# Performance work log

Measured on AMD Instinct MI355X. Metric: run time of the kernel, lower is better.

The kernel has to match this reference:

```python
import jax, jax.numpy as jnp
import numpy as np

L1, L2, N, C = 4096, 4096, 8, 3


def setup_inputs() -> dict:
    key = jax.random.key(0)
    k1, k2 = jax.random.split(key)
    coords1 = jax.random.uniform(k1, (L1, N, C), dtype=jnp.float32)
    coords2 = jax.random.uniform(k2, (L2, N, C), dtype=jnp.float32)
    return {"coords1": coords1, "coords2": coords2}


def reference(coords1, coords2):
    # coords1: [L1, N, C], coords2: [L2, N, C]
    l1, n, c = coords1.shape
    l2 = coords2.shape[0]
    # Batch-first layout, matching flatten_batch semantics (per-batch NN only)
    q = jnp.swapaxes(coords2, 0, 1)  # [N, L2, C] query points
    r = jnp.swapaxes(coords1, 0, 1)  # [N, L1, C] reference points
    # Squared euclidean distances per batch: [N, L2, L1]
    d2 = (
        jnp.sum(q * q, axis=-1)[:, :, None]
        + jnp.sum(r * r, axis=-1)[:, None, :]
        - 2.0 * jnp.einsum("nlc,nmc->nlm", q, r)
    )
    # tc.nearest returns global flat index; original does fmod(L1) to get the
    # per-batch index — argmin within each batch gives that directly.
    nearest = jnp.argmin(d2, axis=-1)  # [N, L2]
    clusters = nearest.T  # [L2, N]
    # torch.meshgrid(arange(L2), arange(N)) with 'ij' indexing; indices[-1] is
    # the batch index broadcast to [L2, N].
    batch_idx = jnp.broadcast_to(jnp.arange(n, dtype=jnp.int64 if False else jnp.int32), (l2, n))
    return (clusters.reshape(-1), batch_idx.reshape(-1))
```

## Files before the change

kernel.cpp:

```cpp
#include <hip/hip_runtime.h>
#include <float.h>


typedef float v2f __attribute__((ext_vector_type(2)));

constexpr int kL1 = 4096, kL2 = 4096, kN = 8;
constexpr int kChunk = 2048;
constexpr int kQPerBlock = 32;

__global__ __launch_bounds__(256, 4)
void nearest_kernel(const float* __restrict__ c1, const float* __restrict__ c2,
                    int* __restrict__ out) {
#pragma clang fp contract(off)
  __shared__ float4 refs[kChunk];

  const int tid = threadIdx.x;
  const int n = blockIdx.y;

  const int g = tid >> 4;
  const int lane16 = tid & 15;
  const int qa = blockIdx.x * kQPerBlock + g * 2;
  const int qb = qa + 1;

  const float* pa = c2 + (qa * kN + n) * 3;
  const float* pb = c2 + (qb * kN + n) * 3;
  const v2f qx = {pa[0], pb[0]};
  const v2f qy = {pa[1], pb[1]};
  const v2f qz = {pa[2], pb[2]};
  const v2f qq = {
      __fadd_rn(__fadd_rn(__fmul_rn(qx.x, qx.x), __fmul_rn(qy.x, qy.x)),
                __fmul_rn(qz.x, qz.x)),
      __fadd_rn(__fadd_rn(__fmul_rn(qx.y, qx.y), __fmul_rn(qy.y, qy.y)),
                __fmul_rn(qz.y, qz.y))};

  v2f bd0 = {FLT_MAX, FLT_MAX}, bd1 = {FLT_MAX, FLT_MAX};
  int bi0a = 0, bi0b = 0, bi1a = 0, bi1b = 0;

  for (int chunk = 0; chunk < kL1 / kChunk; ++chunk) {
    __syncthreads();

#pragma unroll
    for (int k = 0; k < kChunk / 256; ++k) {
      const int j = tid + 256 * k;
      const float* p = c1 + ((chunk * kChunk + j) * kN + n) * 3;
      const float r0 = p[0], r1 = p[1], r2 = p[2];
      const float rr = __fadd_rn(
          __fadd_rn(__fmul_rn(r0, r0), __fmul_rn(r1, r1)), __fmul_rn(r2, r2));
      refs[j] = make_float4(r0, r1, r2, rr);
    }
    __syncthreads();

    const int base = chunk * kChunk;
#pragma unroll 2
    for (int t = 0; t < kChunk / 32; ++t) {
      const int j0 = lane16 + 32 * t;
      const float4 rA = refs[j0];
      const float4 rB = refs[j0 + 16];
      {
        const v2f m0 = qx * rA.x;
        const v2f m1 = qy * rA.y;
        const v2f s01 = m0 + m1;
        const v2f m2 = qz * rA.z;
        const v2f dot = s01 + m2;
        const v2f A = qq + rA.w;
        const float da = __fmaf_rn(-2.0f, dot.x, A.x);
        const float db = __fmaf_rn(-2.0f, dot.y, A.y);
        if (da < bd0.x) { bd0.x = da; bi0a = base + j0; }
        if (db < bd0.y) { bd0.y = db; bi0b = base + j0; }
      }
      {
        const v2f m0 = qx * rB.x;
        const v2f m1 = qy * rB.y;
        const v2f s01 = m0 + m1;
        const v2f m2 = qz * rB.z;
        const v2f dot = s01 + m2;
        const v2f A = qq + rB.w;
        const float da = __fmaf_rn(-2.0f, dot.x, A.x);
        const float db = __fmaf_rn(-2.0f, dot.y, A.y);
        if (da < bd1.x) { bd1.x = da; bi1a = base + j0 + 16; }
        if (db < bd1.y) { bd1.y = db; bi1b = base + j0 + 16; }
      }
    }
  }

  float bda = bd0.x; int bia = bi0a;
  if (bd1.x < bda || (bd1.x == bda && bi1a < bia)) { bda = bd1.x; bia = bi1a; }
  float bdb = bd0.y; int bib = bi0b;
  if (bd1.y < bdb || (bd1.y == bdb && bi1b < bib)) { bdb = bd1.y; bib = bi1b; }

#pragma unroll
  for (int m = 1; m <= 8; m <<= 1) {
    const float oda = __shfl_xor(bda, m);
    const int oia = __shfl_xor(bia, m);
    if (oda < bda || (oda == bda && oia < bia)) { bda = oda; bia = oia; }
    const float odb = __shfl_xor(bdb, m);
    const int oib = __shfl_xor(bib, m);
    if (odb < bdb || (odb == bdb && oib < bib)) { bdb = odb; bib = oib; }
  }

  if (lane16 == 0) {
    out[qa * kN + n] = bia;
    out[qb * kN + n] = bib;
    out[kL2 * kN + qa * kN + n] = n;
    out[kL2 * kN + qb * kN + n] = n;
  }
}

extern "C" void kernel_launch(void* const* d_in, const int* in_sizes, int n_in,
                              void* d_out, int out_size, void* d_ws, size_t ws_size,
                              hipStream_t stream) {
  const float* c1 = (const float*)d_in[0];
  const float* c2 = (const float*)d_in[1];
  int* out = (int*)d_out;
  dim3 grid(kL2 / kQPerBlock, kN);
  nearest_kernel<<<grid, dim3(256), 0, stream>>>(c1, c2, out);
}
```

Baseline: 89.34 us.

## Give each wave 8 queries and stride references across 64 lanes

Work is now split per wavefront: each lane holds 8 queries in registers and walks the reference chunk with stride 64, so every shared-memory load of a reference point feeds 8 distance computations instead of 2. This cuts LDS traffic per distance. In exchange it raises register pressure and makes the final argmin reduction longer, with 6 shuffle steps across 64 lanes for each of 8 queries.

```diff
diff --git a/kernel.cpp b/kernel.cpp
--- a/kernel.cpp
+++ b/kernel.cpp
@@ -6,6 +6,7 @@
 
 constexpr int kL1 = 4096, kL2 = 4096, kN = 8;
 constexpr int kChunk = 2048;
+constexpr int kQ = 8;
 constexpr int kQPerBlock = 32;
 
 __global__ __launch_bounds__(256, 4)
@@ -16,25 +17,33 @@
 
   const int tid = threadIdx.x;
   const int n = blockIdx.y;
+  const int wave = tid >> 6;
+  const int lane = tid & 63;
+  const int q0 = blockIdx.x * kQPerBlock + wave * kQ;
 
-  const int g = tid >> 4;
-  const int lane16 = tid & 15;
-  const int qa = blockIdx.x * kQPerBlock + g * 2;
-  const int qb = qa + 1;
+  v2f qx[4], qy[4], qz[4], qq[4];
+#pragma unroll
+  for (int i = 0; i < 4; ++i) {
+    const float* p0 = c2 + ((q0 + 2 * i) * kN + n) * 3;
+    const float* p1 = c2 + ((q0 + 2 * i + 1) * kN + n) * 3;
+    const float a0 = p0[0], a1 = p0[1], a2 = p0[2];
+    const float b0 = p1[0], b1 = p1[1], b2 = p1[2];
+    qx[i] = v2f{a0, b0};
+    qy[i] = v2f{a1, b1};
+    qz[i] = v2f{a2, b2};
+    qq[i] = v2f{
+        __fadd_rn(__fadd_rn(__fmul_rn(a0, a0), __fmul_rn(a1, a1)),
+                  __fmul_rn(a2, a2)),
+        __fadd_rn(__fadd_rn(__fmul_rn(b0, b0), __fmul_rn(b1, b1)),
+                  __fmul_rn(b2, b2))};
+  }
 
-  const float* pa = c2 + (qa * kN + n) * 3;
-  const float* pb = c2 + (qb * kN + n) * 3;
-  const v2f qx = {pa[0], pb[0]};
-  const v2f qy = {pa[1], pb[1]};
-  const v2f qz = {pa[2], pb[2]};
-  const v2f qq = {
-      __fadd_rn(__fadd_rn(__fmul_rn(qx.x, qx.x), __fmul_rn(qy.x, qy.x)),
-                __fmul_rn(qz.x, qz.x)),
-      __fadd_rn(__fadd_rn(__fmul_rn(qx.y, qx.y), __fmul_rn(qy.y, qy.y)),
-                __fmul_rn(qz.y, qz.y))};
-
-  v2f bd0 = {FLT_MAX, FLT_MAX}, bd1 = {FLT_MAX, FLT_MAX};
-  int bi0a = 0, bi0b = 0, bi1a = 0, bi1b = 0;
+  v2f bd[4];
+  int bi[kQ];
+#pragma unroll
+  for (int i = 0; i < 4; ++i) { bd[i] = v2f{FLT_MAX, FLT_MAX}; }
+#pragma unroll
+  for (int i = 0; i < kQ; ++i) { bi[i] = 0; }
 
   for (int chunk = 0; chunk < kL1 / kChunk; ++chunk) {
     __syncthreads();
@@ -50,59 +59,47 @@
     }
     __syncthreads();
 
-    const int base = chunk * kChunk;
+    const int base = chunk * kChunk + lane;
 #pragma unroll 2
-    for (int t = 0; t < kChunk / 32; ++t) {
-      const int j0 = lane16 + 32 * t;
-      const float4 rA = refs[j0];
-      const float4 rB = refs[j0 + 16];
-      {
-        const v2f m0 = qx * rA.x;
-        const v2f m1 = qy * rA.y;
+    for (int t = 0; t < kChunk / 64; ++t) {
+      const float4 r = refs[lane + 64 * t];
+      const int j = base + 64 * t;
+#pragma unroll
+      for (int i = 0; i < 4; ++i) {
+        const v2f m0 = qx[i] * r.x;
+        const v2f m1 = qy[i] * r.y;
         const v2f s01 = m0 + m1;
-        const v2f m2 = qz * rA.z;
+        const v2f m2 = qz[i] * r.z;
         const v2f dot = s01 + m2;
-        const v2f A = qq + rA.w;
+        const v2f A = qq[i] + r.w;
         const float da = __fmaf_rn(-2.0f, dot.x, A.x);
         const float db = __fmaf_rn(-2.0f, dot.y, A.y);
-        if (da < bd0.x) { bd0.x = da; bi0a = base + j0; }
-        if (db < bd0.y) { bd0.y = db; bi0b = base + j0; }
-      }
-      {
-        const v2f m0 = qx * rB.x;
-        const v2f m1 = qy * rB.y;
-        const v2f s01 = m0 + m1;
-        const v2f m2 = qz * rB.z;
-        const v2f dot = s01 + m2;
-        const v2f A = qq + rB.w;
-        const float da = __fmaf_rn(-2.0f, dot.x, A.x);
-        const float db = __fmaf_rn(-2.0f, dot.y, A.y);
-        if (da < bd1.x) { bd1.x = da; bi1a = base + j0 + 16; }
-        if (db < bd1.y) { bd1.y = db; bi1b = base + j0 + 16; }
+        if (da < bd[i].x) { bd[i].x = da; bi[2 * i] = j; }
+        if (db < bd[i].y) { bd[i].y = db; bi[2 * i + 1] = j; }
       }
     }
   }
 
-  float bda = bd0.x; int bia = bi0a;
-  if (bd1.x < bda || (bd1.x == bda && bi1a < bia)) { bda = bd1.x; bia = bi1a; }
-  float bdb = bd0.y; int bib = bi0b;
-  if (bd1.y < bdb || (bd1.y == bdb && bi1b < bib)) { bdb = bd1.y; bib = bi1b; }
+  float d[kQ];
+#pragma unroll
+  for (int i = 0; i < 4; ++i) { d[2 * i] = bd[i].x; d[2 * i + 1] = bd[i].y; }
 
 #pragma unroll
-  for (int m = 1; m <= 8; m <<= 1) {
-    const float oda = __shfl_xor(bda, m);
-    const int oia = __shfl_xor(bia, m);
-    if (oda < bda || (oda == bda && oia < bia)) { bda = oda; bia = oia; }
-    const float odb = __shfl_xor(bdb, m);
-    const int oib = __shfl_xor(bib, m);
-    if (odb < bdb || (odb == bdb && oib < bib)) { bdb = odb; bib = oib; }
+  for (int i = 0; i < kQ; ++i) {
+#pragma unroll
+    for (int m = 1; m <= 32; m <<= 1) {
+      const float od = __shfl_xor(d[i], m);
+      const int oi = __shfl_xor(bi[i], m);
+      if (od < d[i] || (od == d[i] && oi < bi[i])) { d[i] = od; bi[i] = oi; }
+    }
   }
 
-  if (lane16 == 0) {
-    out[qa * kN + n] = bia;
-    out[qb * kN + n] = bib;
-    out[kL2 * kN + qa * kN + n] = n;
-    out[kL2 * kN + qb * kN + n] = n;
+  if (lane == 0) {
+#pragma unroll
+    for (int i = 0; i < kQ; ++i) {
+      out[(q0 + i) * kN + n] = bi[i];
+      out[kL2 * kN + (q0 + i) * kN + n] = n;
+    }
   }
 }
 
```

After: 94.80 us. 1.06x slower.
